# Kernel tuning notes

Hardware: AMD Instinct MI355X
Metric: run time of the kernel (lower is better)

Reference implementation:

```python
import jax, jax.numpy as jnp
import numpy as np

BS, D, N, E, L, NE = 8, 512, 2048, 8, 64, 524288


def conv1d_same(x, w, b):
    # x: [B, W, Cin], w: [K, Cin, Cout] -> [B, W, Cout], stride 1, 'same' padding
    y = jax.lax.conv_general_dilated(x, w, window_strides=(1,), padding='SAME',
                                     dimension_numbers=('NWC', 'WIO', 'NWC'))
    return y + b


def setup_inputs() -> dict:
    key = jax.random.key(0)
    ks = jax.random.split(key, 10)
    def nrm(k, shape, s=1.0):
        return jax.random.normal(k, shape, jnp.float32) * s
    return {
        'latent': nrm(ks[0], (BS, D)),
        'edge_index': jax.random.randint(ks[1], (2, NE), 0, BS * N),
        'W_dense': nrm(ks[2], (D, N), 0.05),
        'b_dense': jnp.zeros((N,), jnp.float32),
        'conv1_w': nrm(ks[3], (3, 1, E), 0.3),
        'conv1_b': jnp.zeros((E,), jnp.float32),
        'gat_Wq': nrm(ks[4], (E, E), 0.3),
        'gat_bq': jnp.zeros((E,), jnp.float32),
        'gat_Wk': nrm(ks[5], (E, E), 0.3),
        'gat_bk': jnp.zeros((E,), jnp.float32),
        'gat_Wv': nrm(ks[6], (E, E), 0.3),
        'gat_bias': jnp.zeros((E,), jnp.float32),
        'qkv_w': nrm(ks[7], (3, E, 3 * E * L), 0.1),
        'qkv_b': jnp.zeros((3 * E * L,), jnp.float32),
    }


def reference(latent, edge_index, W_dense, b_dense, conv1_w, conv1_b,
              gat_Wq, gat_bq, gat_Wk, gat_bk, gat_Wv, gat_bias, qkv_w, qkv_b):
    bs = latent.shape[0]
    # Dense -> [bs, N], expand -> Conv1D(E) -> [bs, N, E]
    skeleton = latent @ W_dense + b_dense
    skeleton = conv1d_same(skeleton[..., None], conv1_w, conv1_b)
    # concat(unstack, axis=0) == reshape to batched graph nodes [bs*N, E]
    x = skeleton.reshape(bs * N, E)
    BN = bs * N
    # GAT (tf_geometric, num_heads=1): add self-loops, per-edge dot-attention,
    # segment softmax over destination (row), scatter-sum aggregate.
    loops = jnp.arange(BN)
    row = jnp.concatenate([edge_index[0], loops])
    col = jnp.concatenate([edge_index[1], loops])
    Q = jax.nn.leaky_relu(x @ gat_Wq + gat_bq, 0.2)
    K = jax.nn.leaky_relu(x @ gat_Wk + gat_bk, 0.2)
    V = x @ gat_Wv
    score = jnp.sum(Q[row] * K[col], axis=-1)            # [n_edges + BN]
    smax = jax.ops.segment_max(score, row, num_segments=BN)
    ex = jnp.exp(score - smax[row])
    ssum = jax.ops.segment_sum(ex, row, num_segments=BN)
    alpha = ex / ssum[row]                               # segment softmax
    h = jax.ops.segment_sum(alpha[:, None] * V[col], row, num_segments=BN) + gat_bias
    graph = h.reshape(bs, N, E)                          # stack(split(., bs))
    # QVK conv over node axis -> [bs, N, 3*E*L]
    qvk = conv1d_same(graph, qkv_w, qkv_b)
    # stack(split(., L, -1), 1) then concat(unstack(., -2), -1)
    qvk = qvk.reshape(bs, N, L, 3 * E).transpose(0, 2, 1, 3).reshape(bs, L, N * 3 * E)
    q, v, k = jnp.split(qvk, 3, axis=-1)                 # each [bs, L, N*E]
    # keras Attention (use_scale=False): softmax(q @ k^T) @ v
    attn = jax.nn.softmax(jnp.einsum('btd,bsd->bts', q, k), axis=-1)
    seq = jnp.einsum('bts,bsd->btd', attn, v)
    # stack(split(., N, -1), -2) == reshape [bs, L, N, E]
    return seq.reshape(bs, L, N, E)
```

## Files before the change

### kernel.cpp

```cpp
#include <hip/hip_runtime.h>
#include <hip/hip_bf16.h>
#include <math.h>

#define BSZ 8
#define DDIM 512
#define NND 2048
#define EE 8
#define LLH 64
#define NEDGE 524288
#define BNN 16384
#define OCC 1536
#define DQ 16384
#define NCHK 22

typedef __attribute__((ext_vector_type(8))) short short8;
typedef __attribute__((ext_vector_type(4))) float f32x4;

__device__ inline unsigned short f2bf(float x) {
    __hip_bfloat16 h = __float2bfloat16(x);
    return __builtin_bit_cast(unsigned short, h);
}
__device__ inline float bf2f(unsigned short u) {
    return __uint_as_float(((unsigned int)u) << 16);
}

__global__ __launch_bounds__(256) void k_densep(const float* __restrict__ latent,
                                                const float* __restrict__ Wd,
                                                float* __restrict__ pdense,
                                                int* __restrict__ hist) {
    int n0 = blockIdx.x * 32, d0 = blockIdx.y * 64;
    __shared__ float lat[8][64];
    int tid = threadIdx.x;
    if (blockIdx.y == 0) hist[blockIdx.x * 256 + tid] = 0;
    #pragma unroll
    for (int r = 0; r < 2; ++r) {
        int i = r * 256 + tid;
        lat[i >> 6][i & 63] = latent[(i >> 6) * DDIM + d0 + (i & 63)];
    }
    __syncthreads();
    int nl = tid & 31, b = tid >> 5;
    const float* wp = Wd + (size_t)d0 * NND + n0 + nl;
    float acc = 0.f;
    #pragma unroll 8
    for (int d = 0; d < 64; ++d) acc += lat[b][d] * wp[(size_t)d * NND];
    pdense[((size_t)blockIdx.y * BSZ + b) * NND + n0 + nl] = acc;
}

__global__ __launch_bounds__(64) void k_gat(const float* __restrict__ pdense,
                                            const float* __restrict__ bd,
                                            const float* __restrict__ w1,
                                            const float* __restrict__ b1,
                                            const float* __restrict__ Wq, const float* __restrict__ bq,
                                            const float* __restrict__ Wk, const float* __restrict__ bk,
                                            const float* __restrict__ Wv,
                                            const int* __restrict__ ei,
                                            float* __restrict__ Qg, float* __restrict__ Kg,
                                            float* __restrict__ Vg, int* __restrict__ hist) {
    int i = blockIdx.x * 64 + threadIdx.x;
    int b = i >> 11, n = i & (NND - 1);
    float sm = 0.f, s0 = 0.f, sp = 0.f;
    #pragma unroll
    for (int ds = 0; ds < 8; ++ds) {
        const float* p = pdense + ((size_t)ds * BSZ + b) * NND + n;
        if (n > 0) sm += p[-1];
        s0 += p[0];
        if (n < NND - 1) sp += p[1];
    }
    if (n > 0) sm += bd[n - 1];
    s0 += bd[n];
    if (n < NND - 1) sp += bd[n + 1];
    float xr[EE];
    #pragma unroll
    for (int e = 0; e < EE; ++e)
        xr[e] = sm * w1[e] + s0 * w1[EE + e] + sp * w1[2 * EE + e] + b1[e];
    #pragma unroll
    for (int j = 0; j < EE; ++j) {
        float q = bq[j], k = bk[j], v = 0.f;
        #pragma unroll
        for (int c = 0; c < EE; ++c) {
            q += xr[c] * Wq[c * EE + j];
            k += xr[c] * Wk[c * EE + j];
            v += xr[c] * Wv[c * EE + j];
        }
        Qg[(size_t)i * EE + j] = (q >= 0.f) ? q : 0.2f * q;
        Kg[(size_t)i * EE + j] = (k >= 0.f) ? k : 0.2f * k;
        Vg[(size_t)i * EE + j] = v;
    }
    #pragma unroll 4
    for (int j = 0; j < 32; ++j)
        atomicAdd(hist + ei[i + j * BNN], 1);
}

__global__ __launch_bounds__(1024) void k_scan(const int* __restrict__ hist,
                                               int* __restrict__ offs,
                                               int* __restrict__ cnt) {
    int tid = threadIdx.x;
    int lane = tid & 63, wv = tid >> 6;
    const int4* hp = (const int4*)(hist + tid * 16);
    int4 a = hp[0], b4 = hp[1], c4 = hp[2], d4 = hp[3];
    int h[16] = {a.x, a.y, a.z, a.w, b4.x, b4.y, b4.z, b4.w,
                 c4.x, c4.y, c4.z, c4.w, d4.x, d4.y, d4.z, d4.w};
    int mysum = 0;
    #pragma unroll
    for (int i = 0; i < 16; ++i) mysum += h[i];
    int inc = mysum;
    #pragma unroll
    for (int off = 1; off < 64; off <<= 1) {
        int u = __shfl_up(inc, off, 64);
        if (lane >= off) inc += u;
    }
    __shared__ int wtot[16];
    if (lane == 63) wtot[wv] = inc;
    __syncthreads();
    if (tid < 16) {
        int t = wtot[tid];
        #pragma unroll
        for (int off = 1; off < 16; off <<= 1) {
            int u = __shfl_up(t, off, 16);
            if (tid >= off) t += u;
        }
        wtot[tid] = t;
    }
    __syncthreads();
    int run = (wv ? wtot[wv - 1] : 0) + inc - mysum;
    #pragma unroll
    for (int i = 0; i < 16; ++i) {
        offs[tid * 16 + i] = run;
        cnt[tid * 16 + i] = run;
        run += h[i];
    }
}

__global__ void k_scatter(const int* __restrict__ ei, int* __restrict__ cnt,
                          int* __restrict__ ecol) {
    int e = blockIdx.x * 256 + threadIdx.x;
    if (e >= NEDGE) return;
    int r = ei[e], c = ei[NEDGE + e];
    int pos = atomicAdd(cnt + r, 1);
    ecol[pos] = c;
}

__global__ __launch_bounds__(256) void k_gatagg(const int* __restrict__ ecol,
                                                const int* __restrict__ offs,
                                                const int* __restrict__ hist,
                                                const float* __restrict__ Qg,
                                                const float* __restrict__ Kg,
                                                const float* __restrict__ Vg,
                                                const float* __restrict__ gbias,
                                                float* __restrict__ hg) {
    int row = __builtin_amdgcn_readfirstlane(blockIdx.x * 4 + (threadIdx.x >> 6));
    int lane = threadIdx.x & 63;
    const float* Qr = Qg + (size_t)row * EE;
    float q0 = Qr[0], q1 = Qr[1], q2 = Qr[2], q3 = Qr[3];
    float q4 = Qr[4], q5 = Qr[5], q6 = Qr[6], q7 = Qr[7];
    int beg = offs[row], deg = hist[row];
    int total = deg + 1;
    float m = -INFINITY, l = 0.f;
    float acc[EE];
    #pragma unroll
    for (int j = 0; j < EE; ++j) acc[j] = 0.f;
    for (int base = 0; base < total; base += 64) {
        int idx = base + lane;
        int c = row;
        if (idx < deg) c = ecol[beg + idx];
        const float4* K4 = (const float4*)(Kg + (size_t)c * EE);
        float4 ka = K4[0], kb = K4[1];
        float s = q0*ka.x + q1*ka.y + q2*ka.z + q3*ka.w
                + q4*kb.x + q5*kb.y + q6*kb.z + q7*kb.w;
        if (idx >= total) s = -INFINITY;
        float pm = s;
        #pragma unroll
        for (int off = 32; off > 0; off >>= 1) pm = fmaxf(pm, __shfl_xor(pm, off));
        float nm = fmaxf(m, pm);
        float scale = __expf(m - nm);
        float p = (idx < total) ? __expf(s - nm) : 0.f;
        float ps = p;
        #pragma unroll
        for (int off = 32; off > 0; off >>= 1) ps += __shfl_xor(ps, off);
        l = l * scale + ps;
        const float4* V4 = (const float4*)(Vg + (size_t)c * EE);
        float4 va = V4[0], vb = V4[1];
        float pv[EE] = {p*va.x, p*va.y, p*va.z, p*va.w, p*vb.x, p*vb.y, p*vb.z, p*vb.w};
        #pragma unroll
        for (int j = 0; j < EE; ++j) {
            float t = pv[j];
            #pragma unroll
            for (int off = 32; off > 0; off >>= 1) t += __shfl_xor(t, off);
            acc[j] = acc[j] * scale + t;
        }
        m = nm;
    }
    if (lane < EE)
        hg[(size_t)row * EE + lane] = acc[lane] / l + gbias[lane];
}

__global__ __launch_bounds__(256) void k_qkvF(const float* __restrict__ hg,
                                              const float* __restrict__ qw,
                                              const float* __restrict__ qb,
                                              unsigned short* __restrict__ Fq) {
    int n0 = blockIdx.x * 32;
    int b = blockIdx.y;
    __shared__ float hs[34 * EE];
    __shared__ unsigned short st[32 * 768];
    int tid = threadIdx.x;
    for (int i = tid; i < 34 * EE; i += 256) {
        int nn = n0 - 1 + (i >> 3);
        hs[i] = (nn >= 0 && nn < NND) ? hg[((size_t)b * NND + nn) * EE + (i & 7)] : 0.f;
    }
    __syncthreads();
    #pragma unroll
    for (int pass = 0; pass < 2; ++pass) {
        if (pass) __syncthreads();
        float w[3][24], bias[3];
        #pragma unroll
        for (int rr = 0; rr < 3; ++rr) {
            int o = pass * 768 + rr * 256 + tid;
            bias[rr] = qb[o];
            #pragma unroll
            for (int kk = 0; kk < 24; ++kk) w[rr][kk] = qw[kk * OCC + o];
        }
        for (int nn = 0; nn < 32; ++nn) {
            const float* hv = &hs[nn * EE];
            float a0 = bias[0], a1 = bias[1], a2 = bias[2];
            #pragma unroll
            for (int kk = 0; kk < 24; ++kk) {
                float h = hv[kk];
                a0 += h * w[0][kk]; a1 += h * w[1][kk]; a2 += h * w[2][kk];
            }
            st[nn * 768 + tid]       = f2bf(a0);
            st[nn * 768 + tid + 256] = f2bf(a1);
            st[nn * 768 + tid + 512] = f2bf(a2);
        }
        __syncthreads();
        unsigned short* dstbase = Fq + ((size_t)b * NND + n0) * OCC + pass * 768;
        #pragma unroll
        for (int it = 0; it < 12; ++it) {
            int idx8 = it * 256 + tid;
            int row = idx8 / 96, col8 = idx8 - row * 96;
            *(short8*)(dstbase + (size_t)row * OCC + col8 * 8) =
                *(const short8*)(&st[row * 768 + col8 * 8]);
        }
    }
}

__global__ __launch_bounds__(256) void k_attnS(const unsigned short* __restrict__ Fq,
                                               float* __restrict__ Spart) {
    int ch = blockIdx.x, b = blockIdx.y;
    __shared__ unsigned short qt[64 * 200];
    __shared__ unsigned short kt[64 * 200];
    int tid = threadIdx.x;
    int t = tid & 63, nl0 = tid >> 6;
    const unsigned short* Fb = Fq + (size_t)b * NND * OCC;
    short8 z = {0,0,0,0,0,0,0,0};
    int lane = tid & 63, wv = tid >> 6;
    int fr = lane & 15, fk = (lane >> 4) * 8;
    f32x4 accs[4] = {{0,0,0,0},{0,0,0,0},{0,0,0,0},{0,0,0,0}};
    for (int sub = 0; sub < 4; ++sub) {
        int n0 = ch * 32 + sub * 8;
        if (sub) __syncthreads();
        #pragma unroll
        for (int h = 0; h < 2; ++h) {
            int nl = nl0 + h * 4;
            int n = n0 + nl;
            short8 q0 = z, q1 = z, q2 = z;
            if (n <= 682) {
                const short8* p = (const short8*)(Fb + (size_t)n * OCC + t * 24);
                q0 = p[0]; q1 = p[1];
                if (n < 682) q2 = p[2];
            }
            *(short8*)(&qt[t * 200 + nl * 24 + 0])  = q0;
            *(short8*)(&qt[t * 200 + nl * 24 + 8])  = q1;
            *(short8*)(&qt[t * 200 + nl * 24 + 16]) = q2;
            short8 k0 = z, k1 = z, k2 = z;
            if (n <= 682) {
                const short8* p = (const short8*)(Fb + (size_t)(n + 1365) * OCC + t * 24 + 8);
                k0 = p[0]; k1 = p[1];
            }
            if (n <= 681) {
                const short8* p2 = (const short8*)(Fb + (size_t)(n + 1366) * OCC + t * 24);
                k2 = p2[0];
            }
            *(short8*)(&kt[t * 200 + nl * 24 + 0])  = k0;
            *(short8*)(&kt[t * 200 + nl * 24 + 8])  = k1;
            *(short8*)(&kt[t * 200 + nl * 24 + 16]) = k2;
        }
        __syncthreads();
        short8 afr[6];
        #pragma unroll
        for (int ks = 0; ks < 6; ++ks)
            afr[ks] = *(const short8*)(&qt[(wv * 16 + fr) * 200 + ks * 32 + fk]);
        #pragma unroll
        for (int srow = 0; srow < 4; ++srow) {
            #pragma unroll
            for (int ks = 0; ks < 6; ++ks) {
                short8 bfr = *(const short8*)(&kt[(srow * 16 + fr) * 200 + ks * 32 + fk]);
                accs[srow] = __builtin_amdgcn_mfma_f32_16x16x32_bf16(afr[ks], bfr, accs[srow], 0, 0, 0);
            }
        }
    }
    #pragma unroll
    for (int srow = 0; srow < 4; ++srow) {
        float* dst = Spart + (((size_t)ch * BSZ + b) * LLH + wv * 16 + (lane >> 4) * 4) * LLH
                   + srow * 16 + fr;
        #pragma unroll
        for (int r = 0; r < 4; ++r) dst[r * LLH] = accs[srow][r];
    }
}

__global__ void k_softmax(const float* __restrict__ Spart, float* __restrict__ atT) {
    int b = blockIdx.x >> 6, t = blockIdx.x & 63;
    int s = threadIdx.x;
    float v = 0.f;
    for (int ch = 0; ch < NCHK; ++ch)
        v += Spart[(((size_t)ch * BSZ + b) * LLH + t) * LLH + s];
    float m = v;
    #pragma unroll
    for (int off = 32; off > 0; off >>= 1) m = fmaxf(m, __shfl_xor(m, off));
    float e = __expf(v - m);
    float sum = e;
    #pragma unroll
    for (int off = 32; off > 0; off >>= 1) sum += __shfl_xor(sum, off);
    atT[((size_t)b * LLH + s) * LLH + t] = e / sum;
}

__global__ __launch_bounds__(256) void k_attnV(const unsigned short* __restrict__ Fq,
                                               const float* __restrict__ atT,
                                               float* __restrict__ out) {
    int b = blockIdx.y;
    int d0 = blockIdx.x * 64;
    int tid = threadIdx.x;
    __shared__ unsigned short vt[64 * 64];
    const unsigned short* Fb = Fq + (size_t)b * NND * OCC;
    #pragma unroll
    for (int r = 0; r < 16; ++r) {
        int idx = r * 256 + tid;
        int s = idx >> 6, d = idx & 63;
        int f = DQ + d0 + d;
        int n = f / 24, c = f - n * 24;
        vt[s * 64 + d] = Fb[(size_t)n * OCC + s * 24 + c];
    }
    __syncthreads();
    int lane = tid & 63;
    int t0 = __builtin_amdgcn_readfirstlane((tid >> 6) * 16);
    const float* arow = atT + (size_t)b * LLH * LLH + t0;
    float acc[16];
    #pragma unroll
    for (int tt = 0; tt < 16; ++tt) acc[tt] = 0.f;
    #pragma unroll 4
    for (int s = 0; s < LLH; ++s) {
        float vv = bf2f(vt[s * 64 + lane]);
        #pragma unroll
        for (int tt = 0; tt < 16; ++tt)
            acc[tt] += arow[s * LLH + tt] * vv;
    }
    float* ob = out + ((size_t)b * LLH + t0) * DQ + d0 + lane;
    #pragma unroll
    for (int tt = 0; tt < 16; ++tt) ob[(size_t)tt * DQ] = acc[tt];
}

extern "C" void kernel_launch(void* const* d_in, const int* in_sizes, int n_in,
                              void* d_out, int out_size, void* d_ws, size_t ws_size,
                              hipStream_t stream) {
    (void)in_sizes; (void)n_in; (void)out_size; (void)ws_size;
    const float* latent = (const float*)d_in[0];
    const int*   ei     = (const int*)d_in[1];
    const float* Wd     = (const float*)d_in[2];
    const float* bd     = (const float*)d_in[3];
    const float* w1     = (const float*)d_in[4];
    const float* b1     = (const float*)d_in[5];
    const float* Wq     = (const float*)d_in[6];
    const float* bq     = (const float*)d_in[7];
    const float* Wk     = (const float*)d_in[8];
    const float* bk     = (const float*)d_in[9];
    const float* Wv     = (const float*)d_in[10];
    const float* gbias  = (const float*)d_in[11];
    const float* qw     = (const float*)d_in[12];
    const float* qb     = (const float*)d_in[13];
    float* out = (float*)d_out;

    float* ws     = (float*)d_ws;
    float* pdense = ws;
    float* Qg     = pdense + 64 * NND;
    float* Kg     = Qg + BNN * EE;
    float* Vg     = Kg + BNN * EE;
    float* hg     = Vg + BNN * EE;
    int*   hist   = (int*)(hg + BNN * EE);
    int*   offs   = hist + BNN;
    int*   cnt    = offs + BNN;
    int*   ecol   = cnt + BNN;
    float* Spart  = (float*)(ecol + NEDGE);
    float* atT    = Spart + (size_t)NCHK * BSZ * LLH * LLH;
    unsigned short* Fq = (unsigned short*)(atT + BSZ * LLH * LLH);

    k_densep<<<dim3(64, 8), dim3(256), 0, stream>>>(latent, Wd, pdense, hist);
    k_gat<<<dim3(256), dim3(64), 0, stream>>>(pdense, bd, w1, b1, Wq, bq, Wk, bk, Wv,
                                              ei, Qg, Kg, Vg, hist);
    k_scan<<<dim3(1), dim3(1024), 0, stream>>>(hist, offs, cnt);
    k_scatter<<<dim3(NEDGE / 256), dim3(256), 0, stream>>>(ei, cnt, ecol);
    k_gatagg<<<dim3(BNN / 4), dim3(256), 0, stream>>>(ecol, offs, hist,
                                                      Qg, Kg, Vg, gbias, hg);
    k_qkvF<<<dim3(64, 8), dim3(256), 0, stream>>>(hg, qw, qb, Fq);
    k_attnS<<<dim3(NCHK, 8), dim3(256), 0, stream>>>(Fq, Spart);
    k_softmax<<<dim3(512), dim3(64), 0, stream>>>(Spart, atT);
    k_attnV<<<dim3(256, 8), dim3(256), 0, stream>>>(Fq, atT, out);
}
```

Measured before the change: 142.0 us.

## Compute attention scores via low-rank hidden-state Gram matrices instead of materialized Q/K

Rather than materializing the q and k projections in bf16 and multiplying them with MFMA, the code builds small 25x25 Gram-like moments of the shifted GAT outputs (plus ones for bias) per batch. It then contracts these with the conv weights in a new fused score-plus-softmax kernel. Only the v portion of the projection (nodes 682..1365) is still written to Fq, which cuts projection writes and score-kernel reads. The trade-off is more intricate index algebra and fp32 reductions with a different summation order, and the final kernel runs on only 64 blocks.

```diff
diff --git a/kernel.cpp b/kernel.cpp
--- a/kernel.cpp
+++ b/kernel.cpp
@@ -11,10 +11,8 @@
 #define BNN 16384
 #define OCC 1536
 #define DQ 16384
-#define NCHK 22
 
 typedef __attribute__((ext_vector_type(8))) short short8;
-typedef __attribute__((ext_vector_type(4))) float f32x4;
 
 __device__ inline unsigned short f2bf(float x) {
     __hip_bfloat16 h = __float2bfloat16(x);
@@ -194,133 +192,161 @@
         hg[(size_t)row * EE + lane] = acc[lane] / l + gbias[lane];
 }
 
-__global__ __launch_bounds__(256) void k_qkvF(const float* __restrict__ hg,
-                                              const float* __restrict__ qw,
-                                              const float* __restrict__ qb,
-                                              unsigned short* __restrict__ Fq) {
-    int n0 = blockIdx.x * 32;
-    int b = blockIdx.y;
-    __shared__ float hs[34 * EE];
-    __shared__ unsigned short st[32 * 768];
-    int tid = threadIdx.x;
-    for (int i = tid; i < 34 * EE; i += 256) {
-        int nn = n0 - 1 + (i >> 3);
-        hs[i] = (nn >= 0 && nn < NND) ? hg[((size_t)b * NND + nn) * EE + (i & 7)] : 0.f;
-    }
-    __syncthreads();
-    #pragma unroll
-    for (int pass = 0; pass < 2; ++pass) {
-        if (pass) __syncthreads();
-        float w[3][24], bias[3];
-        #pragma unroll
-        for (int rr = 0; rr < 3; ++rr) {
-            int o = pass * 768 + rr * 256 + tid;
-            bias[rr] = qb[o];
+__global__ __launch_bounds__(256) void k_qkvFvM(const float* __restrict__ hg,
+                                                const float* __restrict__ qw,
+                                                const float* __restrict__ qb,
+                                                unsigned short* __restrict__ Fq,
+                                                float* __restrict__ Mpart) {
+    int bx = blockIdx.x, b = blockIdx.y, tid = threadIdx.x;
+    if (bx < 22) {
+        int n0 = 682 + bx * 32;
+        __shared__ float hs[34 * EE];
+        __shared__ unsigned short st[32 * 768];
+        for (int i = tid; i < 34 * EE; i += 256) {
+            int nn = n0 - 1 + (i >> 3);
+            hs[i] = (nn >= 0 && nn < NND) ? hg[((size_t)b * NND + nn) * EE + (i & 7)] : 0.f;
+        }
+        __syncthreads();
+        #pragma unroll
+        for (int pass = 0; pass < 2; ++pass) {
+            if (pass) __syncthreads();
+            float w[3][24], bias[3];
             #pragma unroll
-            for (int kk = 0; kk < 24; ++kk) w[rr][kk] = qw[kk * OCC + o];
-        }
-        for (int nn = 0; nn < 32; ++nn) {
-            const float* hv = &hs[nn * EE];
-            float a0 = bias[0], a1 = bias[1], a2 = bias[2];
+            for (int rr = 0; rr < 3; ++rr) {
+                int o = pass * 768 + rr * 256 + tid;
+                bias[rr] = qb[o];
+                #pragma unroll
+                for (int kk = 0; kk < 24; ++kk) w[rr][kk] = qw[kk * OCC + o];
+            }
+            for (int nn = 0; nn < 32; ++nn) {
+                const float* hv = &hs[nn * EE];
+                float a0 = bias[0], a1 = bias[1], a2 = bias[2];
+                #pragma unroll
+                for (int kk = 0; kk < 24; ++kk) {
+                    float h = hv[kk];
+                    a0 += h * w[0][kk]; a1 += h * w[1][kk]; a2 += h * w[2][kk];
+                }
+                st[nn * 768 + tid]       = f2bf(a0);
+                st[nn * 768 + tid + 256] = f2bf(a1);
+                st[nn * 768 + tid + 512] = f2bf(a2);
+            }
+            __syncthreads();
+            unsigned short* dstbase = Fq + ((size_t)b * NND + n0) * OCC + pass * 768;
             #pragma unroll
-            for (int kk = 0; kk < 24; ++kk) {
-                float h = hv[kk];
-                a0 += h * w[0][kk]; a1 += h * w[1][kk]; a2 += h * w[2][kk];
+            for (int it = 0; it < 12; ++it) {
+                int idx8 = it * 256 + tid;
+                int row = idx8 / 96, col8 = idx8 - row * 96;
+                if (n0 + row <= 1365)
+                    *(short8*)(dstbase + (size_t)row * OCC + col8 * 8) =
+                        *(const short8*)(&st[row * 768 + col8 * 8]);
             }
-            st[nn * 768 + tid]       = f2bf(a0);
-            st[nn * 768 + tid + 256] = f2bf(a1);
-            st[nn * 768 + tid + 512] = f2bf(a2);
+        }
+    } else {
+        int sp = bx - 22;
+        int nq0 = sp * 86;
+        __shared__ float hq[88][EE];
+        __shared__ float hk[90][EE];
+        for (int i = tid; i < 88 * EE; i += 256) {
+            int r = nq0 - 1 + (i >> 3);
+            hq[i >> 3][i & 7] = (r >= 0 && r < NND) ? hg[((size_t)b * NND + r) * EE + (i & 7)] : 0.f;
+        }
+        for (int i = tid; i < 90 * EE; i += 256) {
+            int r = nq0 + 1364 + (i >> 3);
+            hk[i >> 3][i & 7] = (r < NND) ? hg[((size_t)b * NND + r) * EE + (i & 7)] : 0.f;
         }
         __syncthreads();
-        unsigned short* dstbase = Fq + ((size_t)b * NND + n0) * OCC + pass * 768;
-        #pragma unroll
-        for (int it = 0; it < 12; ++it) {
-            int idx8 = it * 256 + tid;
-            int row = idx8 / 96, col8 = idx8 - row * 96;
-            *(short8*)(dstbase + (size_t)row * OCC + col8 * 8) =
-                *(const short8*)(&st[row * 768 + col8 * 8]);
-        }
-    }
-}
-
-__global__ __launch_bounds__(256) void k_attnS(const unsigned short* __restrict__ Fq,
-                                               float* __restrict__ Spart) {
-    int ch = blockIdx.x, b = blockIdx.y;
-    __shared__ unsigned short qt[64 * 200];
-    __shared__ unsigned short kt[64 * 200];
-    int tid = threadIdx.x;
-    int t = tid & 63, nl0 = tid >> 6;
-    const unsigned short* Fb = Fq + (size_t)b * NND * OCC;
-    short8 z = {0,0,0,0,0,0,0,0};
-    int lane = tid & 63, wv = tid >> 6;
-    int fr = lane & 15, fk = (lane >> 4) * 8;
-    f32x4 accs[4] = {{0,0,0,0},{0,0,0,0},{0,0,0,0},{0,0,0,0}};
-    for (int sub = 0; sub < 4; ++sub) {
-        int n0 = ch * 32 + sub * 8;
-        if (sub) __syncthreads();
-        #pragma unroll
-        for (int h = 0; h < 2; ++h) {
-            int nl = nl0 + h * 4;
-            int n = n0 + nl;
-            short8 q0 = z, q1 = z, q2 = z;
-            if (n <= 682) {
-                const short8* p = (const short8*)(Fb + (size_t)n * OCC + t * 24);
-                q0 = p[0]; q1 = p[1];
-                if (n < 682) q2 = p[2];
+        int cnt1 = 683 - nq0; if (cnt1 > 86) cnt1 = 86; if (cnt1 < 0) cnt1 = 0;
+        int cnt2 = 682 - nq0; if (cnt2 > 86) cnt2 = 86; if (cnt2 < 0) cnt2 = 0;
+        for (int idx = tid; idx < 1250; idx += 256) {
+            int mm = idx / 625, p = idx - (idx / 625) * 625;
+            int i = p / 25, j = p - (p / 25) * 25;
+            int cnt = mm ? cnt2 : cnt1;
+            int qi = i >> 3, qe = i & 7;
+            int kj = (j >> 3) + mm, ke = j & 7;
+            float acc = 0.f;
+            if (i < 24 && j < 24) {
+                for (int nl = 0; nl < cnt; ++nl)
+                    acc += hq[nl + qi][qe] * hk[nl + kj][ke];
+            } else if (i < 24) {
+                for (int nl = 0; nl < cnt; ++nl) acc += hq[nl + qi][qe];
+            } else if (j < 24) {
+                for (int nl = 0; nl < cnt; ++nl) acc += hk[nl + kj][ke];
+            } else {
+                acc = (float)cnt;
             }
-            *(short8*)(&qt[t * 200 + nl * 24 + 0])  = q0;
-            *(short8*)(&qt[t * 200 + nl * 24 + 8])  = q1;
-            *(short8*)(&qt[t * 200 + nl * 24 + 16]) = q2;
-            short8 k0 = z, k1 = z, k2 = z;
-            if (n <= 682) {
-                const short8* p = (const short8*)(Fb + (size_t)(n + 1365) * OCC + t * 24 + 8);
-                k0 = p[0]; k1 = p[1];
-            }
-            if (n <= 681) {
-                const short8* p2 = (const short8*)(Fb + (size_t)(n + 1366) * OCC + t * 24);
-                k2 = p2[0];
-            }
-            *(short8*)(&kt[t * 200 + nl * 24 + 0])  = k0;
-            *(short8*)(&kt[t * 200 + nl * 24 + 8])  = k1;
-            *(short8*)(&kt[t * 200 + nl * 24 + 16]) = k2;
-        }
-        __syncthreads();
-        short8 afr[6];
-        #pragma unroll
-        for (int ks = 0; ks < 6; ++ks)
-            afr[ks] = *(const short8*)(&qt[(wv * 16 + fr) * 200 + ks * 32 + fk]);
-        #pragma unroll
-        for (int srow = 0; srow < 4; ++srow) {
-            #pragma unroll
-            for (int ks = 0; ks < 6; ++ks) {
-                short8 bfr = *(const short8*)(&kt[(srow * 16 + fr) * 200 + ks * 32 + fk]);
-                accs[srow] = __builtin_amdgcn_mfma_f32_16x16x32_bf16(afr[ks], bfr, accs[srow], 0, 0, 0);
-            }
-        }
-    }
-    #pragma unroll
-    for (int srow = 0; srow < 4; ++srow) {
-        float* dst = Spart + (((size_t)ch * BSZ + b) * LLH + wv * 16 + (lane >> 4) * 4) * LLH
-                   + srow * 16 + fr;
-        #pragma unroll
-        for (int r = 0; r < 4; ++r) dst[r * LLH] = accs[srow][r];
-    }
-}
-
-__global__ void k_softmax(const float* __restrict__ Spart, float* __restrict__ atT) {
-    int b = blockIdx.x >> 6, t = blockIdx.x & 63;
-    int s = threadIdx.x;
-    float v = 0.f;
-    for (int ch = 0; ch < NCHK; ++ch)
-        v += Spart[(((size_t)ch * BSZ + b) * LLH + t) * LLH + s];
-    float m = v;
-    #pragma unroll
-    for (int off = 32; off > 0; off >>= 1) m = fmaxf(m, __shfl_xor(m, off));
-    float e = __expf(v - m);
-    float sum = e;
-    #pragma unroll
-    for (int off = 32; off > 0; off >>= 1) sum += __shfl_xor(sum, off);
-    atT[((size_t)b * LLH + s) * LLH + t] = e / sum;
+            Mpart[((size_t)(sp * 8 + b)) * 1250 + idx] = acc;
+        }
+    }
+}
+
+__global__ __launch_bounds__(256) void k_Ssm(const float* __restrict__ qw,
+                                             const float* __restrict__ qb,
+                                             const float* __restrict__ Mpart,
+                                             float* __restrict__ atT) {
+    __shared__ float Ms[8][1250];
+    __shared__ float As[25 * 24];
+    __shared__ float T1[8][25 * 24];
+    int t = blockIdx.x, tid = threadIdx.x;
+    for (int idx = tid; idx < 10000; idx += 256) {
+        int b = idx / 1250, r = idx - (idx / 1250) * 1250;
+        float s = 0.f;
+        #pragma unroll
+        for (int sp = 0; sp < 8; ++sp)
+            s += Mpart[((size_t)(sp * 8 + b)) * 1250 + r];
+        Ms[b][r] = s;
+    }
+    for (int idx = tid; idx < 600; idx += 256) {
+        int i = idx / 24, c = idx - (idx / 24) * 24;
+        As[idx] = (i < 24) ? qw[i * OCC + t * 24 + c] : qb[t * 24 + c];
+    }
+    __syncthreads();
+    for (int idx = tid; idx < 4800; idx += 256) {
+        int b = idx / 600, rem = idx - (idx / 600) * 600;
+        int j = rem / 24, c = rem - (rem / 24) * 24;
+        int mo = (c < 16) ? 0 : 625;
+        float acc = 0.f;
+        #pragma unroll 5
+        for (int i = 0; i < 25; ++i)
+            acc += Ms[b][mo + i * 25 + j] * As[i * 24 + c];
+        T1[b][j * 24 + c] = acc;
+    }
+    __syncthreads();
+    int s = tid & 63, bg = tid >> 6;
+    float acc0 = 0.f, acc1 = 0.f;
+    for (int j = 0; j < 25; ++j) {
+        float Bv[24];
+        const float* bp = (j < 24) ? (qw + (size_t)j * OCC + s * 24) : (qb + s * 24);
+        #pragma unroll
+        for (int r = 0; r < 6; ++r) {
+            float4 v = *(const float4*)(bp + r * 4);
+            Bv[r*4+0]=v.x; Bv[r*4+1]=v.y; Bv[r*4+2]=v.z; Bv[r*4+3]=v.w;
+        }
+        const float* t1a = &T1[bg][j * 24];
+        const float* t1b = &T1[bg + 4][j * 24];
+        #pragma unroll
+        for (int c = 0; c < 16; ++c) {
+            acc0 += t1a[c] * Bv[8 + c];
+            acc1 += t1b[c] * Bv[8 + c];
+        }
+        #pragma unroll
+        for (int c = 16; c < 24; ++c) {
+            acc0 += t1a[c] * Bv[c - 16];
+            acc1 += t1b[c] * Bv[c - 16];
+        }
+    }
+    #pragma unroll
+    for (int r = 0; r < 2; ++r) {
+        int b = bg + r * 4;
+        float v = r ? acc1 : acc0;
+        float m = v;
+        #pragma unroll
+        for (int off = 32; off > 0; off >>= 1) m = fmaxf(m, __shfl_xor(m, off));
+        float e = __expf(v - m);
+        float sum = e;
+        #pragma unroll
+        for (int off = 32; off > 0; off >>= 1) sum += __shfl_xor(sum, off);
+        atT[((size_t)b * LLH + s) * LLH + t] = e / sum;
+    }
 }
 
 __global__ __launch_bounds__(256) void k_attnV(const unsigned short* __restrict__ Fq,
@@ -388,8 +414,8 @@
     int*   offs   = hist + BNN;
     int*   cnt    = offs + BNN;
     int*   ecol   = cnt + BNN;
-    float* Spart  = (float*)(ecol + NEDGE);
-    float* atT    = Spart + (size_t)NCHK * BSZ * LLH * LLH;
+    float* Mp     = (float*)(ecol + NEDGE);
+    float* atT    = Mp + 80000;
     unsigned short* Fq = (unsigned short*)(atT + BSZ * LLH * LLH);
 
     k_densep<<<dim3(64, 8), dim3(256), 0, stream>>>(latent, Wd, pdense, hist);
@@ -399,8 +425,7 @@
     k_scatter<<<dim3(NEDGE / 256), dim3(256), 0, stream>>>(ei, cnt, ecol);
     k_gatagg<<<dim3(BNN / 4), dim3(256), 0, stream>>>(ecol, offs, hist,
                                                       Qg, Kg, Vg, gbias, hg);
-    k_qkvF<<<dim3(64, 8), dim3(256), 0, stream>>>(hg, qw, qb, Fq);
-    k_attnS<<<dim3(NCHK, 8), dim3(256), 0, stream>>>(Fq, Spart);
-    k_softmax<<<dim3(512), dim3(64), 0, stream>>>(Spart, atT);
+    k_qkvFvM<<<dim3(30, 8), dim3(256), 0, stream>>>(hg, qw, qb, Fq, Mp);
+    k_Ssm<<<dim3(64), dim3(256), 0, stream>>>(qw, qb, Mp, atT);
     k_attnV<<<dim3(256, 8), dim3(256), 0, stream>>>(Fq, atT, out);
 }
```

Result: slower. 148.2 us (+4.3%).
